# Optimization experiments

Hardware: AMD Instinct MI355X
Metric: run time of the kernel (lower is better)

The kernel has to match this reference:

```python
import jax, jax.numpy as jnp
import numpy as np

HEADS = 24
HEAD_DIM = 128
COND = 1024      # (512//8)*(512//8)*16//64
TXTLEN = 128
EPS = 1e-6


def setup_inputs() -> dict:
    key = jax.random.key(0)
    ks = jax.random.split(key, 16)
    S, D, R = 2176, 3072, 16
    f = lambda k, shp, s=1.0: jax.random.normal(k, shp, dtype=jnp.float32) * s
    return {
        "hidden_states": f(ks[0], (1, S, D)),
        "Wq": f(ks[1], (D, D), 0.02), "bq": f(ks[2], (D,), 0.02),
        "Wk": f(ks[3], (D, D), 0.02), "bk": f(ks[4], (D,), 0.02),
        "Wv": f(ks[5], (D, D), 0.02), "bv": f(ks[6], (D,), 0.02),
        "q_down": f(ks[7], (R, D), 1.0 / R), "q_up": f(ks[8], (D, R), 0.02),
        "k_down": f(ks[9], (R, D), 1.0 / R), "k_up": f(ks[10], (D, R), 0.02),
        "v_down": f(ks[11], (R, D), 1.0 / R), "v_up": f(ks[12], (D, R), 0.02),
        "norm_q_w": jnp.ones((HEAD_DIM,), jnp.float32),
        "norm_k_w": jnp.ones((HEAD_DIM,), jnp.float32),
        "rope_cos": f(ks[13], (S, HEAD_DIM)),
        "rope_sin": f(ks[14], (S, HEAD_DIM)),
    }


def _rms_norm(x, w):
    # per-head RMSNorm over head_dim
    var = jnp.mean(x * x, axis=-1, keepdims=True)
    return x * jax.lax.rsqrt(var + EPS) * w


def _apply_rope(x, cos, sin):
    # diffusers apply_rotary_emb, use_real=True, unbind_dim=-1 (interleaved pairs)
    xr = x.reshape(*x.shape[:-1], HEAD_DIM // 2, 2)
    x_rot = jnp.stack([-xr[..., 1], xr[..., 0]], axis=-1).reshape(x.shape)
    return x * cos[None, None] + x_rot * sin[None, None]


def _forward(hidden_states, Wq, bq, Wk, bk, Wv, bv,
             q_down, q_up, k_down, k_up, v_down, v_up,
             norm_q_w, norm_k_w, rope_cos, rope_sin):
    B, S, D = hidden_states.shape
    block = S - COND  # scaled_block_size

    # dense QKV projections
    q = hidden_states @ Wq.T + bq
    k = hidden_states @ Wk.T + bk
    v = hidden_states @ Wv.T + bv

    # LoRA on cond segment only (mask zeros all rows outside [block, block+COND))
    pos = jnp.arange(S)
    seg = ((pos >= block) & (pos < block + COND)).astype(hidden_states.dtype)[None, :, None]
    hm = hidden_states * seg
    # lora_weight=1.0, network_alpha/rank = 16/16 = 1.0
    q = q + (hm @ q_down.T) @ q_up.T
    k = k + (hm @ k_down.T) @ k_up.T
    v = v + (hm @ v_down.T) @ v_up.T

    # [B, H, S, hd]
    to_heads = lambda t: t.reshape(B, S, HEADS, HEAD_DIM).transpose(0, 2, 1, 3)
    q, k, v = to_heads(q), to_heads(k), to_heads(v)

    q = _rms_norm(q, norm_q_w)
    k = _rms_norm(k, norm_k_w)

    q = _apply_rope(q, rope_cos, rope_sin)
    k = _apply_rope(k, rope_cos, rope_sin)

    # additive mask: rows < block attend everything; cond rows (n_loras=1)
    # attend only their own cond block
    row, col = pos[:, None], pos[None, :]
    allowed = (row < block) | ((row >= block) & (col >= block))
    bias = jnp.where(allowed, 0.0, -1e20).astype(q.dtype)

    scale = 1.0 / np.sqrt(HEAD_DIM)
    scores = jnp.einsum("bhqd,bhkd->bhqk", q, k) * scale + bias
    attn = jax.nn.softmax(scores, axis=-1)
    out = jnp.einsum("bhqk,bhkd->bhqd", attn, v)

    out = out.transpose(0, 2, 1, 3).reshape(B, S, HEADS * HEAD_DIM)
    return out[:, :block, :]  # hidden_states (use_cond=False)


def reference(hidden_states, Wq, bq, Wk, bk, Wv, bv,
              q_down, q_up, k_down, k_up, v_down, v_up,
              norm_q_w, norm_k_w, rope_cos, rope_sin):
    return _forward(hidden_states, Wq, bq, Wk, bk, Wv, bv,
                    q_down, q_up, k_down, k_up, v_down, v_up,
                    norm_q_w, norm_k_w, rope_cos, rope_sin)
```

## Files before the change

kernel.cpp:

```cpp
#include <hip/hip_runtime.h>
#include <stdint.h>

#define Sq   2176
#define Dm   3072
#define NDm  9216
#define NH   24
#define HDm  128
#define BLKR 1152
#define KVH  1088
#define NT2  34

typedef __attribute__((ext_vector_type(8))) __bf16 bf16x8;
typedef __attribute__((ext_vector_type(4))) float f32x4;
typedef __attribute__((ext_vector_type(8))) unsigned short ushort8;

#define AS1 __attribute__((address_space(1)))
#define AS3 __attribute__((address_space(3)))

__device__ __forceinline__ unsigned short f2bf(float x) {
  unsigned u = __builtin_bit_cast(unsigned, x);
  u += 0x7FFFu + ((u >> 16) & 1u);
  return (unsigned short)(u >> 16);
}

__global__ void cvt_kernel(const float* __restrict__ src,
                           unsigned short* __restrict__ dst, int n8) {
  int i = blockIdx.x * blockDim.x + threadIdx.x;
  if (i >= n8) return;
  const float4* s4 = (const float4*)src + (size_t)i * 2;
  float4 a = s4[0], b = s4[1];
  ushort8 o;
  o[0]=f2bf(a.x); o[1]=f2bf(a.y); o[2]=f2bf(a.z); o[3]=f2bf(a.w);
  o[4]=f2bf(b.x); o[5]=f2bf(b.y); o[6]=f2bf(b.z); o[7]=f2bf(b.w);
  *((ushort8*)dst + i) = o;
}

__global__ void cvt3_kernel(const float* __restrict__ w0, const float* __restrict__ w1,
                            const float* __restrict__ w2,
                            unsigned short* __restrict__ dst, int n8) {
  int i = blockIdx.x * blockDim.x + threadIdx.x;
  if (i >= n8) return;
  const float* src = blockIdx.y == 0 ? w0 : (blockIdx.y == 1 ? w1 : w2);
  const float4* s4 = (const float4*)src + (size_t)i * 2;
  float4 a = s4[0], b = s4[1];
  ushort8 o;
  o[0]=f2bf(a.x); o[1]=f2bf(a.y); o[2]=f2bf(a.z); o[3]=f2bf(a.w);
  o[4]=f2bf(b.x); o[5]=f2bf(b.y); o[6]=f2bf(b.z); o[7]=f2bf(b.w);
  *((ushort8*)dst + (size_t)blockIdx.y * (Dm * (size_t)Dm / 8) + i) = o;
}

__global__ __launch_bounds__(256) void lorat_kernel(
    const float* __restrict__ hs,
    const float* __restrict__ k_down, const float* __restrict__ v_down,
    float* __restrict__ tkW, float* __restrict__ tvW) {
  int srow = BLKR + blockIdx.x;
  int t = threadIdx.x;
  __shared__ float hsl[Dm];
  __shared__ float tl[32];
  for (int e = t; e < Dm; e += 256) hsl[e] = hs[(size_t)srow * Dm + e];
  __syncthreads();
  int dot = t >> 3, part = t & 7;
  int mat = dot >> 4, j = dot & 15;
  const float* down = mat ? v_down : k_down;
  float p = 0.f;
  for (int e = part; e < Dm; e += 8) p += hsl[e] * down[j * Dm + e];
  p += __shfl_xor(p, 1, 64);
  p += __shfl_xor(p, 2, 64);
  p += __shfl_xor(p, 4, 64);
  if (part == 0) tl[dot] = p;
  __syncthreads();
  if (t < 16) tkW[(size_t)blockIdx.x * 16 + t] = tl[t];
  else if (t < 32) tvW[(size_t)blockIdx.x * 16 + (t - 16)] = tl[t];
}

__global__ __launch_bounds__(256, 4) void gemm_kernel(
    const unsigned short* __restrict__ A,
    const unsigned short* __restrict__ B,
    const float* __restrict__ bq, const float* __restrict__ bk,
    const float* __restrict__ bv,
    const float* __restrict__ tkW, const float* __restrict__ tvW,
    const float* __restrict__ kup, const float* __restrict__ vup,
    const float* __restrict__ nqw, const float* __restrict__ nkw,
    const float* __restrict__ rc, const float* __restrict__ rs,
    unsigned short* __restrict__ qh, unsigned short* __restrict__ kh,
    unsigned short* __restrict__ vtb) {
  __shared__ __attribute__((aligned(16))) unsigned short sm[17408];
  __shared__ float rsum[2][2][64];
  int t = threadIdx.x;
  int wid = t >> 6, lane = t & 63;
  int lr = lane & 15, lg = lane >> 4;
  int wr = wid >> 1, wc = wid & 1;

  int bid = blockIdx.x;
  int wg = (bid & 7) * 129 + (bid >> 3);
  int mt, nt;
  if (wg < 216) { nt = wg / 9; mt = wg % 9; }
  else { int r2 = wg - 216; nt = 24 + r2 / 17; mt = r2 % 17; }
  int m0 = mt * 128, n0 = nt * 128;

  f32x4 acc[4][4];
#pragma unroll
  for (int m = 0; m < 4; m++)
#pragma unroll
    for (int n = 0; n < 4; n++) acc[m][n] = (f32x4){0.f, 0.f, 0.f, 0.f};

  int tr = t >> 3;
  int uu = (t & 7) ^ (tr & 7);
  const unsigned short* pA = A + (size_t)(m0 + tr) * Dm + uu * 8;
  const unsigned short* pB = B + (size_t)(n0 + tr) * Dm + uu * 8;

  int lr7 = lr & 7;
  int baseA = (wr * 64 + lr) * 64;
  int baseB = (wc * 64 + lr) * 64;
  int d0 = (lg ^ lr7) * 8;
  int d1 = ((4 + lg) ^ lr7) * 8;

  for (int kt = 0; kt < Dm / 64; kt++) {
    const int ko = kt * 64;
#pragma unroll
    for (int c = 0; c < 4; c++) {
      __builtin_amdgcn_global_load_lds(
          (const AS1 void*)(pA + (size_t)c * 32 * Dm + ko),
          (AS3 void*)(&sm[c * 2048 + wid * 512]), 16, 0, 0);
      __builtin_amdgcn_global_load_lds(
          (const AS1 void*)(pB + (size_t)c * 32 * Dm + ko),
          (AS3 void*)(&sm[8192 + c * 2048 + wid * 512]), 16, 0, 0);
    }
    __syncthreads();

    bf16x8 a0[4], b0[4];
#pragma unroll
    for (int m = 0; m < 4; m++) a0[m] = *(const bf16x8*)&sm[baseA + m * 1024 + d0];
#pragma unroll
    for (int n = 0; n < 4; n++) b0[n] = *(const bf16x8*)&sm[8192 + baseB + n * 1024 + d0];
#pragma unroll
    for (int m = 0; m < 4; m++)
#pragma unroll
      for (int n = 0; n < 4; n++)
        acc[m][n] = __builtin_amdgcn_mfma_f32_16x16x32_bf16(a0[m], b0[n], acc[m][n], 0, 0, 0);

    bf16x8 a1[4], b1[4];
#pragma unroll
    for (int m = 0; m < 4; m++) a1[m] = *(const bf16x8*)&sm[baseA + m * 1024 + d1];
#pragma unroll
    for (int n = 0; n < 4; n++) b1[n] = *(const bf16x8*)&sm[8192 + baseB + n * 1024 + d1];
#pragma unroll
    for (int m = 0; m < 4; m++)
#pragma unroll
      for (int n = 0; n < 4; n++)
        acc[m][n] = __builtin_amdgcn_mfma_f32_16x16x32_bf16(a1[m], b1[n], acc[m][n], 0, 0, 0);
    __syncthreads();
  }

  int region = nt < 24 ? 0 : (nt < 48 ? 1 : 2);
  int h = region == 0 ? nt : (region == 1 ? nt - 24 : nt - 48);
  int dcol[4];
#pragma unroll
  for (int n = 0; n < 4; n++) dcol[n] = wc * 64 + n * 16 + lr;
  const float* bias = region == 0 ? bq : (region == 1 ? bk : bv);
#pragma unroll
  for (int n = 0; n < 4; n++) {
    float b = bias[h * 128 + dcol[n]];
#pragma unroll
    for (int m = 0; m < 4; m++)
#pragma unroll
      for (int i = 0; i < 4; i++) acc[m][n][i] += b;
  }

  if (region >= 1 && m0 >= BLKR) {
    const float* tW = region == 1 ? tkW : tvW;
    const float* up = region == 1 ? kup : vup;
    int rr = t >> 1, half = t & 1;
    const float* srcT = tW + ((size_t)(m0 - BLKR) + rr) * 16 + half * 8;
    const float* srcU = up + ((size_t)h * 128 + rr) * 16 + half * 8;
    ushort8 vT, vU;
#pragma unroll
    for (int u2 = 0; u2 < 8; u2++) { vT[u2] = f2bf(srcT[u2]); vU[u2] = f2bf(srcU[u2]); }
    ushort8 z = {0, 0, 0, 0, 0, 0, 0, 0};
    *(ushort8*)&sm[(rr * 8 + (half ^ (rr & 7))) * 8] = vT;
    *(ushort8*)&sm[(rr * 8 + ((2 + half) ^ (rr & 7))) * 8] = z;
    *(ushort8*)&sm[8192 + (rr * 8 + (half ^ (rr & 7))) * 8] = vU;
    *(ushort8*)&sm[8192 + (rr * 8 + ((2 + half) ^ (rr & 7))) * 8] = z;
    __syncthreads();
    bf16x8 a0[4], b0[4];
#pragma unroll
    for (int m = 0; m < 4; m++) a0[m] = *(const bf16x8*)&sm[baseA + m * 1024 + d0];
#pragma unroll
    for (int n = 0; n < 4; n++) b0[n] = *(const bf16x8*)&sm[8192 + baseB + n * 1024 + d0];
#pragma unroll
    for (int m = 0; m < 4; m++)
#pragma unroll
      for (int n = 0; n < 4; n++)
        acc[m][n] = __builtin_amdgcn_mfma_f32_16x16x32_bf16(a0[m], b0[n], acc[m][n], 0, 0, 0);
    __syncthreads();
  }

  if (region <= 1) {
    float part[4][4];
#pragma unroll
    for (int m = 0; m < 4; m++)
#pragma unroll
      for (int i = 0; i < 4; i++) {
        float p = acc[m][0][i] * acc[m][0][i] + acc[m][1][i] * acc[m][1][i]
                + acc[m][2][i] * acc[m][2][i] + acc[m][3][i] * acc[m][3][i];
#pragma unroll
        for (int d = 1; d < 16; d <<= 1) p += __shfl_xor(p, d, 64);
        part[m][i] = p;
      }
    if (lr == 0) {
#pragma unroll
      for (int m = 0; m < 4; m++)
#pragma unroll
        for (int i = 0; i < 4; i++) rsum[wr][wc][m * 16 + lg * 4 + i] = part[m][i];
    }
    __syncthreads();
    const float* nw = region == 0 ? nqw : nkw;
    float wv[4];
#pragma unroll
    for (int n = 0; n < 4; n++) wv[n] = nw[dcol[n]];
    unsigned short* dstb = region == 0 ? qh : kh;
    int srows = region == 0 ? BLKR : Sq;
#pragma unroll
    for (int m = 0; m < 4; m++)
#pragma unroll
      for (int i = 0; i < 4; i++) {
        int idx = m * 16 + lg * 4 + i;
        float s2 = rsum[wr][0][idx] + rsum[wr][1][idx];
        float rinv = rsqrtf(s2 * (1.f / 128.f) + 1e-6f);
        int r = m0 + wr * 64 + idx;
#pragma unroll
        for (int n = 0; n < 4; n++) {
          float xn = acc[m][n][i] * rinv * wv[n];
          float xp = __shfl_xor(xn, 1, 64);
          float c = rc[r * 128 + dcol[n]];
          float s = rs[r * 128 + dcol[n]];
          float rot = (dcol[n] & 1) ? xp : -xp;
          dstb[((size_t)h * srows + r) * 128 + dcol[n]] = f2bf(xn * c + rot * s);
        }
      }
  } else {
#pragma unroll
    for (int m = 0; m < 4; m++)
#pragma unroll
      for (int i = 0; i < 4; i++) {
        int rl = wr * 64 + m * 16 + lg * 4 + i;
#pragma unroll
        for (int n = 0; n < 4; n++)
          sm[dcol[n] * 136 + rl] = f2bf(acc[m][n][i]);
      }
    __syncthreads();
    int d = t >> 1, rc0 = (t & 1) * 64;
    unsigned short* dv = vtb + ((size_t)h * 128 + d) * Sq + m0 + rc0;
#pragma unroll
    for (int u = 0; u < 8; u++)
      *(ushort8*)(dv + u * 8) = *(const ushort8*)&sm[d * 136 + rc0 + u * 8];
  }
}

__global__ __launch_bounds__(256) void attn_kernel(
    const unsigned short* __restrict__ qh,
    const unsigned short* __restrict__ kh,
    const unsigned short* __restrict__ vt,
    float* __restrict__ accW,
    float* __restrict__ lW) {
  int bid = blockIdx.x;
  int wg = (bid & 7) * 108 + (bid >> 3);
  int h = wg / 36, rem = wg % 36;
  int qt = rem >> 1, split = rem & 1;
  int q0 = qt * 64;
  int k0 = split * KVH;

  int t = threadIdx.x;
  int w = t >> 6, lane = t & 63;
  int lr = lane & 15, lg = lane >> 4;

  __shared__ __attribute__((aligned(16))) unsigned short kLds[2][32 * 128];
  __shared__ __attribute__((aligned(16))) unsigned short vLds[2][128 * 32];

  const unsigned short* qb = qh + ((size_t)h * BLKR + q0 + w * 16) * 128;
  bf16x8 aq[4];
#pragma unroll
  for (int m = 0; m < 4; m++)
    aq[m] = *(const bf16x8*)(qb + (size_t)lr * 128 + m * 32 + lg * 8);

  const unsigned short* kh_h = kh + ((size_t)h * Sq + k0) * 128;
  const unsigned short* vt_h = vt + (size_t)h * 128 * Sq + k0;

  const unsigned short* srcK[2];
  const unsigned short* srcV[2];
  int kDst[2], vDst[2];
#pragma unroll
  for (int c = 0; c < 2; c++) {
    int u = c * 256 + t;
    int rK = u >> 4, sK = u & 15;
    srcK[c] = kh_h + (size_t)rK * 128 + ((sK ^ (rK & 7)) * 8);
    kDst[c] = u * 8;
    int rV = u >> 2, sV = u & 3;
    srcV[c] = vt_h + (size_t)rV * Sq + ((sV ^ (rV & 3)) * 8);
    vDst[c] = u * 8;
  }

  auto stage = [&](int kt, int buf) {
#pragma unroll
    for (int c = 0; c < 2; c++)
      __builtin_amdgcn_global_load_lds(
          (const AS1 void*)(srcK[c] + (size_t)kt * 4096),
          (AS3 void*)(&kLds[buf][kDst[c]]), 16, 0, 0);
#pragma unroll
    for (int c = 0; c < 2; c++)
      __builtin_amdgcn_global_load_lds(
          (const AS1 void*)(srcV[c] + (size_t)kt * 32),
          (AS3 void*)(&vLds[buf][vDst[c]]), 16, 0, 0);
  };

  f32x4 acc[8];
#pragma unroll
  for (int o = 0; o < 8; o++) acc[o] = (f32x4){0.f, 0.f, 0.f, 0.f};
  float lsum = 0.f;
  const float sc = 0.08838834764831845f;
  const float L2E = 1.4426950408889634f;
  const float ea = sc * L2E, eb = -10.0f * L2E;

  int lr7 = lr & 7, lr3 = lr & 3;
  int adLo = ((((lg & 1) << 1)) * 16 + lr) * 4;
  int adHi = adLo + 64;
  bool hiKb = (lg & 2) != 0;

  auto compute = [&](int buf) {
    const unsigned short* kbuf = kLds[buf];
    const unsigned short* vbuf = vLds[buf];
    f32x4 s2[2];
    s2[0] = (f32x4){0.f, 0.f, 0.f, 0.f};
    s2[1] = (f32x4){0.f, 0.f, 0.f, 0.f};
    __builtin_amdgcn_s_setprio(1);
#pragma unroll
    for (int kb = 0; kb < 2; kb++)
#pragma unroll
      for (int m = 0; m < 4; m++) {
        bf16x8 kf = *(const bf16x8*)&kbuf[(kb * 16 + lr) * 128 + ((m * 4 + lg) ^ lr7) * 8];
        s2[kb] = __builtin_amdgcn_mfma_f32_16x16x32_bf16(kf, aq[m], s2[kb], 0, 0, 0);
      }
    __builtin_amdgcn_s_setprio(0);
    unsigned pk0[2], pk1[2];
#pragma unroll
    for (int kb = 0; kb < 2; kb++) {
      float p0 = exp2f(fmaf(s2[kb][0], ea, eb));
      float p1 = exp2f(fmaf(s2[kb][1], ea, eb));
      float p2 = exp2f(fmaf(s2[kb][2], ea, eb));
      float p3 = exp2f(fmaf(s2[kb][3], ea, eb));
      lsum += (p0 + p1) + (p2 + p3);
      unsigned r0, r1;
      asm("v_cvt_pk_bf16_f32 %0, %1, %2" : "=v"(r0) : "v"(p0), "v"(p1));
      asm("v_cvt_pk_bf16_f32 %0, %1, %2" : "=v"(r1) : "v"(p2), "v"(p3));
      if (kb == 0) { pk0[0] = r0; pk0[1] = r1; }
      else         { pk1[0] = r0; pk1[1] = r1; }
    }
    int a00 = __builtin_amdgcn_ds_bpermute(adLo, (int)pk0[0]);
    int a01 = __builtin_amdgcn_ds_bpermute(adLo, (int)pk0[1]);
    int a10 = __builtin_amdgcn_ds_bpermute(adLo, (int)pk1[0]);
    int a11 = __builtin_amdgcn_ds_bpermute(adLo, (int)pk1[1]);
    int b00 = __builtin_amdgcn_ds_bpermute(adHi, (int)pk0[0]);
    int b01 = __builtin_amdgcn_ds_bpermute(adHi, (int)pk0[1]);
    int b10 = __builtin_amdgcn_ds_bpermute(adHi, (int)pk1[0]);
    int b11 = __builtin_amdgcn_ds_bpermute(adHi, (int)pk1[1]);
    int4 pw;
    pw.x = hiKb ? a10 : a00;
    pw.y = hiKb ? a11 : a01;
    pw.z = hiKb ? b10 : b00;
    pw.w = hiKb ? b11 : b01;
    bf16x8 pfrag = __builtin_bit_cast(bf16x8, pw);
    __builtin_amdgcn_s_setprio(1);
#pragma unroll
    for (int o = 0; o < 8; o++) {
      bf16x8 vf = *(const bf16x8*)&vbuf[(o * 16 + lr) * 32 + (lg ^ lr3) * 8];
      acc[o] = __builtin_amdgcn_mfma_f32_16x16x32_bf16(vf, pfrag, acc[o], 0, 0, 0);
    }
    __builtin_amdgcn_s_setprio(0);
  };

  stage(0, 0);
  __syncthreads();
  for (int kt = 0; kt < NT2; kt += 2) {
    stage(kt + 1, 1);
    compute(0);
    __syncthreads();
    if (kt + 2 < NT2) stage(kt + 2, 0);
    compute(1);
    __syncthreads();
  }

  lsum += __shfl_xor(lsum, 16, 64);
  lsum += __shfl_xor(lsum, 32, 64);

  float* accP = accW + (size_t)split * BLKR * 3072;
  size_t rowOff = (size_t)(q0 + w * 16 + lr) * 3072 + h * 128;
#pragma unroll
  for (int o = 0; o < 8; o++)
    *(f32x4*)&accP[rowOff + o * 16 + lg * 4] = acc[o];
  if (lg == 0) {
    float* lP = lW + (size_t)split * NH * BLKR + (size_t)h * BLKR;
    lP[q0 + w * 16 + lr] = lsum;
  }
}

__global__ __launch_bounds__(256) void normalize_kernel(
    const float* __restrict__ accW, const float* __restrict__ lW,
    float* __restrict__ out) {
  int idx = blockIdx.x * 256 + threadIdx.x;
  int r = idx / 384, rem = idx % 384;
  int c = rem * 8, h = c >> 7;
  const float4* a0 = (const float4*)(accW + (size_t)r * 3072 + c);
  const float4* a1 = (const float4*)(accW + (size_t)BLKR * 3072 + (size_t)r * 3072 + c);
  float l = lW[(size_t)h * BLKR + r] + lW[(size_t)NH * BLKR + (size_t)h * BLKR + r];
  float inv = 1.0f / l;
  float4 v0 = a0[0], v1 = a0[1], u0 = a1[0], u1 = a1[1];
  float4 o0, o1;
  o0.x = (v0.x + u0.x) * inv; o0.y = (v0.y + u0.y) * inv;
  o0.z = (v0.z + u0.z) * inv; o0.w = (v0.w + u0.w) * inv;
  o1.x = (v1.x + u1.x) * inv; o1.y = (v1.y + u1.y) * inv;
  o1.z = (v1.z + u1.z) * inv; o1.w = (v1.w + u1.w) * inv;
  float4* op = (float4*)(out + (size_t)r * 3072 + c);
  op[0] = o0; op[1] = o1;
}

extern "C" void kernel_launch(void* const* d_in, const int* in_sizes, int n_in,
                              void* d_out, int out_size, void* d_ws, size_t ws_size,
                              hipStream_t stream) {
  const float* hs  = (const float*)d_in[0];
  const float* Wq  = (const float*)d_in[1];
  const float* bq  = (const float*)d_in[2];
  const float* Wk  = (const float*)d_in[3];
  const float* bk  = (const float*)d_in[4];
  const float* Wv  = (const float*)d_in[5];
  const float* bv  = (const float*)d_in[6];
  const float* k_down = (const float*)d_in[9];
  const float* k_up   = (const float*)d_in[10];
  const float* v_down = (const float*)d_in[11];
  const float* v_up   = (const float*)d_in[12];
  const float* nqw = (const float*)d_in[13];
  const float* nkw = (const float*)d_in[14];
  const float* rc  = (const float*)d_in[15];
  const float* rsn = (const float*)d_in[16];
  float* out = (float*)d_out;

  char* ws = (char*)d_ws;
  unsigned short* hsb = (unsigned short*)(ws + 0);
  unsigned short* wb  = (unsigned short*)(ws + 13369344);
  float* accW = (float*)(ws + 69992448);
  float* lW   = (float*)(ws + 98304000);
  float* tkW  = (float*)(ws + 98525184);
  float* tvW  = (float*)(ws + 98590720);
  unsigned short* qh  = (unsigned short*)(ws + 150208512);
  unsigned short* kh  = (unsigned short*)(ws + 157286400);
  unsigned short* vtb = (unsigned short*)(ws + 170655744);

  const int n8_hs = Sq * Dm / 8;
  const int n8_w  = Dm * Dm / 8;
  cvt_kernel<<<dim3((n8_hs + 255) / 256), 256, 0, stream>>>(hs, hsb, n8_hs);
  cvt3_kernel<<<dim3((n8_w + 255) / 256, 3), 256, 0, stream>>>(Wq, Wk, Wv, wb, n8_w);
  lorat_kernel<<<dim3(Sq - BLKR), 256, 0, stream>>>(hs, k_down, v_down, tkW, tvW);

  gemm_kernel<<<dim3(1032), 256, 0, stream>>>(hsb, wb, bq, bk, bv,
                                              tkW, tvW, k_up, v_up,
                                              nqw, nkw, rc, rsn, qh, kh, vtb);
  attn_kernel<<<dim3(2 * 18 * NH), 256, 0, stream>>>(qh, kh, vtb, accW, lW);
  normalize_kernel<<<dim3(BLKR * 3072 / 8 / 256), 256, 0, stream>>>(accW, lW, out);
}
```

Before: 304.0 us.

## Load K/V fragments directly from global memory instead of LDS double-buffering

The attention kernel stops staging K and V tiles into shared memory with async global-to-LDS loads and barriers. Each wave now loads its own K and V MFMA fragments straight from global memory into registers every iteration. This removes the LDS traffic and block-wide syncs, but each of the four waves re-reads the same K/V data from global/L2, and there is no explicit prefetch to hide load latency.

```diff
diff --git a/kernel.cpp b/kernel.cpp
--- a/kernel.cpp
+++ b/kernel.cpp
@@ -274,44 +274,14 @@
   int w = t >> 6, lane = t & 63;
   int lr = lane & 15, lg = lane >> 4;
 
-  __shared__ __attribute__((aligned(16))) unsigned short kLds[2][32 * 128];
-  __shared__ __attribute__((aligned(16))) unsigned short vLds[2][128 * 32];
-
   const unsigned short* qb = qh + ((size_t)h * BLKR + q0 + w * 16) * 128;
   bf16x8 aq[4];
 #pragma unroll
   for (int m = 0; m < 4; m++)
     aq[m] = *(const bf16x8*)(qb + (size_t)lr * 128 + m * 32 + lg * 8);
 
-  const unsigned short* kh_h = kh + ((size_t)h * Sq + k0) * 128;
-  const unsigned short* vt_h = vt + (size_t)h * 128 * Sq + k0;
-
-  const unsigned short* srcK[2];
-  const unsigned short* srcV[2];
-  int kDst[2], vDst[2];
-#pragma unroll
-  for (int c = 0; c < 2; c++) {
-    int u = c * 256 + t;
-    int rK = u >> 4, sK = u & 15;
-    srcK[c] = kh_h + (size_t)rK * 128 + ((sK ^ (rK & 7)) * 8);
-    kDst[c] = u * 8;
-    int rV = u >> 2, sV = u & 3;
-    srcV[c] = vt_h + (size_t)rV * Sq + ((sV ^ (rV & 3)) * 8);
-    vDst[c] = u * 8;
-  }
-
-  auto stage = [&](int kt, int buf) {
-#pragma unroll
-    for (int c = 0; c < 2; c++)
-      __builtin_amdgcn_global_load_lds(
-          (const AS1 void*)(srcK[c] + (size_t)kt * 4096),
-          (AS3 void*)(&kLds[buf][kDst[c]]), 16, 0, 0);
-#pragma unroll
-    for (int c = 0; c < 2; c++)
-      __builtin_amdgcn_global_load_lds(
-          (const AS1 void*)(srcV[c] + (size_t)kt * 32),
-          (AS3 void*)(&vLds[buf][vDst[c]]), 16, 0, 0);
-  };
+  const unsigned short* kp = kh + ((size_t)h * Sq + k0 + lr) * 128 + lg * 8;
+  const unsigned short* vp = vt + ((size_t)h * 128 + lr) * Sq + k0 + lg * 8;
 
   f32x4 acc[8];
 #pragma unroll
@@ -321,14 +291,24 @@
   const float L2E = 1.4426950408889634f;
   const float ea = sc * L2E, eb = -10.0f * L2E;
 
-  int lr7 = lr & 7, lr3 = lr & 3;
   int adLo = ((((lg & 1) << 1)) * 16 + lr) * 4;
   int adHi = adLo + 64;
   bool hiKb = (lg & 2) != 0;
 
-  auto compute = [&](int buf) {
-    const unsigned short* kbuf = kLds[buf];
-    const unsigned short* vbuf = vLds[buf];
+  for (int kt = 0; kt < NT2; kt++) {
+    const unsigned short* kpt = kp + (size_t)kt * 32 * 128;
+    const unsigned short* vpt = vp + kt * 32;
+    bf16x8 kf[2][4];
+#pragma unroll
+    for (int kb = 0; kb < 2; kb++)
+#pragma unroll
+      for (int m = 0; m < 4; m++)
+        kf[kb][m] = *(const bf16x8*)(kpt + kb * 16 * 128 + m * 32);
+    bf16x8 vf[8];
+#pragma unroll
+    for (int o = 0; o < 8; o++)
+      vf[o] = *(const bf16x8*)(vpt + (size_t)o * 16 * Sq);
+
     f32x4 s2[2];
     s2[0] = (f32x4){0.f, 0.f, 0.f, 0.f};
     s2[1] = (f32x4){0.f, 0.f, 0.f, 0.f};
@@ -336,11 +316,10 @@
 #pragma unroll
     for (int kb = 0; kb < 2; kb++)
 #pragma unroll
-      for (int m = 0; m < 4; m++) {
-        bf16x8 kf = *(const bf16x8*)&kbuf[(kb * 16 + lr) * 128 + ((m * 4 + lg) ^ lr7) * 8];
-        s2[kb] = __builtin_amdgcn_mfma_f32_16x16x32_bf16(kf, aq[m], s2[kb], 0, 0, 0);
-      }
+      for (int m = 0; m < 4; m++)
+        s2[kb] = __builtin_amdgcn_mfma_f32_16x16x32_bf16(kf[kb][m], aq[m], s2[kb], 0, 0, 0);
     __builtin_amdgcn_s_setprio(0);
+
     unsigned pk0[2], pk1[2];
 #pragma unroll
     for (int kb = 0; kb < 2; kb++) {
@@ -371,22 +350,9 @@
     bf16x8 pfrag = __builtin_bit_cast(bf16x8, pw);
     __builtin_amdgcn_s_setprio(1);
 #pragma unroll
-    for (int o = 0; o < 8; o++) {
-      bf16x8 vf = *(const bf16x8*)&vbuf[(o * 16 + lr) * 32 + (lg ^ lr3) * 8];
-      acc[o] = __builtin_amdgcn_mfma_f32_16x16x32_bf16(vf, pfrag, acc[o], 0, 0, 0);
-    }
+    for (int o = 0; o < 8; o++)
+      acc[o] = __builtin_amdgcn_mfma_f32_16x16x32_bf16(vf[o], pfrag, acc[o], 0, 0, 0);
     __builtin_amdgcn_s_setprio(0);
-  };
-
-  stage(0, 0);
-  __syncthreads();
-  for (int kt = 0; kt < NT2; kt += 2) {
-    stage(kt + 1, 1);
-    compute(0);
-    __syncthreads();
-    if (kt + 2 < NT2) stage(kt + 2, 0);
-    compute(1);
-    __syncthreads();
   }
 
   lsum += __shfl_xor(lsum, 16, 64);
```

Result: slower. 488.1 us (+60.5%).

## Double attention query tile per workgroup to reuse K/V LDS tiles

Applied to the files above, without the earlier changes.

Each attention workgroup now processes 128 query rows instead of 64, with each wave holding two 16-row Q sub-tiles. Every K and V fragment loaded from LDS feeds two MFMAs, which halves K/V global and LDS traffic per query. The grid shrinks from 864 to 432 workgroups, which lowers occupancy and CU fill on a 256-CU part and raises register pressure from the doubled accumulators.

```diff
diff --git a/kernel.cpp b/kernel.cpp
--- a/kernel.cpp
+++ b/kernel.cpp
@@ -264,10 +264,10 @@
     float* __restrict__ accW,
     float* __restrict__ lW) {
   int bid = blockIdx.x;
-  int wg = (bid & 7) * 108 + (bid >> 3);
-  int h = wg / 36, rem = wg % 36;
+  int wg = (bid & 7) * 54 + (bid >> 3);
+  int h = wg / 18, rem = wg % 18;
   int qt = rem >> 1, split = rem & 1;
-  int q0 = qt * 64;
+  int q0 = qt * 128;
   int k0 = split * KVH;
 
   int t = threadIdx.x;
@@ -277,11 +277,13 @@
   __shared__ __attribute__((aligned(16))) unsigned short kLds[2][32 * 128];
   __shared__ __attribute__((aligned(16))) unsigned short vLds[2][128 * 32];
 
-  const unsigned short* qb = qh + ((size_t)h * BLKR + q0 + w * 16) * 128;
-  bf16x8 aq[4];
-#pragma unroll
-  for (int m = 0; m < 4; m++)
-    aq[m] = *(const bf16x8*)(qb + (size_t)lr * 128 + m * 32 + lg * 8);
+  const unsigned short* qb = qh + ((size_t)h * BLKR + q0 + w * 32) * 128;
+  bf16x8 aq[2][4];
+#pragma unroll
+  for (int qs = 0; qs < 2; qs++)
+#pragma unroll
+    for (int m = 0; m < 4; m++)
+      aq[qs][m] = *(const bf16x8*)(qb + (size_t)(qs * 16 + lr) * 128 + m * 32 + lg * 8);
 
   const unsigned short* kh_h = kh + ((size_t)h * Sq + k0) * 128;
   const unsigned short* vt_h = vt + (size_t)h * 128 * Sq + k0;
@@ -313,10 +315,12 @@
           (AS3 void*)(&vLds[buf][vDst[c]]), 16, 0, 0);
   };
 
-  f32x4 acc[8];
-#pragma unroll
-  for (int o = 0; o < 8; o++) acc[o] = (f32x4){0.f, 0.f, 0.f, 0.f};
-  float lsum = 0.f;
+  f32x4 acc[2][8];
+#pragma unroll
+  for (int qs = 0; qs < 2; qs++)
+#pragma unroll
+    for (int o = 0; o < 8; o++) acc[qs][o] = (f32x4){0.f, 0.f, 0.f, 0.f};
+  float lsum[2] = {0.f, 0.f};
   const float sc = 0.08838834764831845f;
   const float L2E = 1.4426950408889634f;
   const float ea = sc * L2E, eb = -10.0f * L2E;
@@ -329,51 +333,66 @@
   auto compute = [&](int buf) {
     const unsigned short* kbuf = kLds[buf];
     const unsigned short* vbuf = vLds[buf];
-    f32x4 s2[2];
-    s2[0] = (f32x4){0.f, 0.f, 0.f, 0.f};
-    s2[1] = (f32x4){0.f, 0.f, 0.f, 0.f};
+    f32x4 s2[2][2];
+#pragma unroll
+    for (int qs = 0; qs < 2; qs++) {
+      s2[qs][0] = (f32x4){0.f, 0.f, 0.f, 0.f};
+      s2[qs][1] = (f32x4){0.f, 0.f, 0.f, 0.f};
+    }
     __builtin_amdgcn_s_setprio(1);
 #pragma unroll
-    for (int kb = 0; kb < 2; kb++)
-#pragma unroll
-      for (int m = 0; m < 4; m++) {
-        bf16x8 kf = *(const bf16x8*)&kbuf[(kb * 16 + lr) * 128 + ((m * 4 + lg) ^ lr7) * 8];
-        s2[kb] = __builtin_amdgcn_mfma_f32_16x16x32_bf16(kf, aq[m], s2[kb], 0, 0, 0);
+    for (int kb = 0; kb < 2; kb++) {
+      bf16x8 kf[4];
+#pragma unroll
+      for (int m = 0; m < 4; m++)
+        kf[m] = *(const bf16x8*)&kbuf[(kb * 16 + lr) * 128 + ((m * 4 + lg) ^ lr7) * 8];
+#pragma unroll
+      for (int qs = 0; qs < 2; qs++)
+#pragma unroll
+        for (int m = 0; m < 4; m++)
+          s2[qs][kb] = __builtin_amdgcn_mfma_f32_16x16x32_bf16(kf[m], aq[qs][m], s2[qs][kb], 0, 0, 0);
+    }
+    __builtin_amdgcn_s_setprio(0);
+
+    bf16x8 pfrag[2];
+#pragma unroll
+    for (int qs = 0; qs < 2; qs++) {
+      unsigned pk0[2], pk1[2];
+#pragma unroll
+      for (int kb = 0; kb < 2; kb++) {
+        float p0 = exp2f(fmaf(s2[qs][kb][0], ea, eb));
+        float p1 = exp2f(fmaf(s2[qs][kb][1], ea, eb));
+        float p2 = exp2f(fmaf(s2[qs][kb][2], ea, eb));
+        float p3 = exp2f(fmaf(s2[qs][kb][3], ea, eb));
+        lsum[qs] += (p0 + p1) + (p2 + p3);
+        unsigned r0, r1;
+        asm("v_cvt_pk_bf16_f32 %0, %1, %2" : "=v"(r0) : "v"(p0), "v"(p1));
+        asm("v_cvt_pk_bf16_f32 %0, %1, %2" : "=v"(r1) : "v"(p2), "v"(p3));
+        if (kb == 0) { pk0[0] = r0; pk0[1] = r1; }
+        else         { pk1[0] = r0; pk1[1] = r1; }
       }
-    __builtin_amdgcn_s_setprio(0);
-    unsigned pk0[2], pk1[2];
-#pragma unroll
-    for (int kb = 0; kb < 2; kb++) {
-      float p0 = exp2f(fmaf(s2[kb][0], ea, eb));
-      float p1 = exp2f(fmaf(s2[kb][1], ea, eb));
-      float p2 = exp2f(fmaf(s2[kb][2], ea, eb));
-      float p3 = exp2f(fmaf(s2[kb][3], ea, eb));
-      lsum += (p0 + p1) + (p2 + p3);
-      unsigned r0, r1;
-      asm("v_cvt_pk_bf16_f32 %0, %1, %2" : "=v"(r0) : "v"(p0), "v"(p1));
-      asm("v_cvt_pk_bf16_f32 %0, %1, %2" : "=v"(r1) : "v"(p2), "v"(p3));
-      if (kb == 0) { pk0[0] = r0; pk0[1] = r1; }
-      else         { pk1[0] = r0; pk1[1] = r1; }
-    }
-    int a00 = __builtin_amdgcn_ds_bpermute(adLo, (int)pk0[0]);
-    int a01 = __builtin_amdgcn_ds_bpermute(adLo, (int)pk0[1]);
-    int a10 = __builtin_amdgcn_ds_bpermute(adLo, (int)pk1[0]);
-    int a11 = __builtin_amdgcn_ds_bpermute(adLo, (int)pk1[1]);
-    int b00 = __builtin_amdgcn_ds_bpermute(adHi, (int)pk0[0]);
-    int b01 = __builtin_amdgcn_ds_bpermute(adHi, (int)pk0[1]);
-    int b10 = __builtin_amdgcn_ds_bpermute(adHi, (int)pk1[0]);
-    int b11 = __builtin_amdgcn_ds_bpermute(adHi, (int)pk1[1]);
-    int4 pw;
-    pw.x = hiKb ? a10 : a00;
-    pw.y = hiKb ? a11 : a01;
-    pw.z = hiKb ? b10 : b00;
-    pw.w = hiKb ? b11 : b01;
-    bf16x8 pfrag = __builtin_bit_cast(bf16x8, pw);
+      int a00 = __builtin_amdgcn_ds_bpermute(adLo, (int)pk0[0]);
+      int a01 = __builtin_amdgcn_ds_bpermute(adLo, (int)pk0[1]);
+      int a10 = __builtin_amdgcn_ds_bpermute(adLo, (int)pk1[0]);
+      int a11 = __builtin_amdgcn_ds_bpermute(adLo, (int)pk1[1]);
+      int b00 = __builtin_amdgcn_ds_bpermute(adHi, (int)pk0[0]);
+      int b01 = __builtin_amdgcn_ds_bpermute(adHi, (int)pk0[1]);
+      int b10 = __builtin_amdgcn_ds_bpermute(adHi, (int)pk1[0]);
+      int b11 = __builtin_amdgcn_ds_bpermute(adHi, (int)pk1[1]);
+      int4 pw;
+      pw.x = hiKb ? a10 : a00;
+      pw.y = hiKb ? a11 : a01;
+      pw.z = hiKb ? b10 : b00;
+      pw.w = hiKb ? b11 : b01;
+      pfrag[qs] = __builtin_bit_cast(bf16x8, pw);
+    }
+
     __builtin_amdgcn_s_setprio(1);
 #pragma unroll
     for (int o = 0; o < 8; o++) {
       bf16x8 vf = *(const bf16x8*)&vbuf[(o * 16 + lr) * 32 + (lg ^ lr3) * 8];
-      acc[o] = __builtin_amdgcn_mfma_f32_16x16x32_bf16(vf, pfrag, acc[o], 0, 0, 0);
+      acc[0][o] = __builtin_amdgcn_mfma_f32_16x16x32_bf16(vf, pfrag[0], acc[0][o], 0, 0, 0);
+      acc[1][o] = __builtin_amdgcn_mfma_f32_16x16x32_bf16(vf, pfrag[1], acc[1][o], 0, 0, 0);
     }
     __builtin_amdgcn_s_setprio(0);
   };
@@ -389,17 +408,24 @@
     __syncthreads();
   }
 
-  lsum += __shfl_xor(lsum, 16, 64);
-  lsum += __shfl_xor(lsum, 32, 64);
+#pragma unroll
+  for (int qs = 0; qs < 2; qs++) {
+    lsum[qs] += __shfl_xor(lsum[qs], 16, 64);
+    lsum[qs] += __shfl_xor(lsum[qs], 32, 64);
+  }
 
   float* accP = accW + (size_t)split * BLKR * 3072;
-  size_t rowOff = (size_t)(q0 + w * 16 + lr) * 3072 + h * 128;
-#pragma unroll
-  for (int o = 0; o < 8; o++)
-    *(f32x4*)&accP[rowOff + o * 16 + lg * 4] = acc[o];
+#pragma unroll
+  for (int qs = 0; qs < 2; qs++) {
+    size_t rowOff = (size_t)(q0 + w * 32 + qs * 16 + lr) * 3072 + h * 128;
+#pragma unroll
+    for (int o = 0; o < 8; o++)
+      *(f32x4*)&accP[rowOff + o * 16 + lg * 4] = acc[qs][o];
+  }
   if (lg == 0) {
     float* lP = lW + (size_t)split * NH * BLKR + (size_t)h * BLKR;
-    lP[q0 + w * 16 + lr] = lsum;
+    lP[q0 + w * 32 + lr] = lsum[0];
+    lP[q0 + w * 32 + 16 + lr] = lsum[1];
   }
 }
 
@@ -463,6 +489,6 @@
   gemm_kernel<<<dim3(1032), 256, 0, stream>>>(hsb, wb, bq, bk, bv,
                                               tkW, tvW, k_up, v_up,
                                               nqw, nkw, rc, rsn, qh, kh, vtb);
-  attn_kernel<<<dim3(2 * 18 * NH), 256, 0, stream>>>(qh, kh, vtb, accW, lW);
+  attn_kernel<<<dim3(2 * 9 * NH), 256, 0, stream>>>(qh, kh, vtb, accW, lW);
   normalize_kernel<<<dim3(BLKR * 3072 / 8 / 256), 256, 0, stream>>>(accW, lW, out);
 }
```

New measurement: 313.0 us. +2.9%, slower.

## Fuse prep kernels into one launch and store split-attention partials in bf16

Applied to the files above, without the earlier changes.

Merges the hidden-state conversion, the three weight conversions and the LoRA down-projection into a single prep kernel. The LoRA part now handles four rows per block so each down-projection load is reused four times. The attention kernel writes its split-K partial accumulators as bf16 instead of fp32, halving partial-output traffic, and the normalize kernel reads them back as bf16. This removes two launches and some memory traffic, at the cost of extra rounding error in the partial sums.

```diff
diff --git a/kernel.cpp b/kernel.cpp
--- a/kernel.cpp
+++ b/kernel.cpp
@@ -9,6 +9,11 @@
 #define BLKR 1152
 #define KVH  1088
 #define NT2  34
+#define N8HS 835584
+#define N8W  1179648
+#define NB_CVT   3264
+#define NB_W     13824
+#define NB_LORAT 256
 
 typedef __attribute__((ext_vector_type(8))) __bf16 bf16x8;
 typedef __attribute__((ext_vector_type(4))) float f32x4;
@@ -22,55 +27,75 @@
   u += 0x7FFFu + ((u >> 16) & 1u);
   return (unsigned short)(u >> 16);
 }
-
-__global__ void cvt_kernel(const float* __restrict__ src,
-                           unsigned short* __restrict__ dst, int n8) {
-  int i = blockIdx.x * blockDim.x + threadIdx.x;
-  if (i >= n8) return;
-  const float4* s4 = (const float4*)src + (size_t)i * 2;
-  float4 a = s4[0], b = s4[1];
-  ushort8 o;
-  o[0]=f2bf(a.x); o[1]=f2bf(a.y); o[2]=f2bf(a.z); o[3]=f2bf(a.w);
-  o[4]=f2bf(b.x); o[5]=f2bf(b.y); o[6]=f2bf(b.z); o[7]=f2bf(b.w);
-  *((ushort8*)dst + i) = o;
-}
-
-__global__ void cvt3_kernel(const float* __restrict__ w0, const float* __restrict__ w1,
-                            const float* __restrict__ w2,
-                            unsigned short* __restrict__ dst, int n8) {
-  int i = blockIdx.x * blockDim.x + threadIdx.x;
-  if (i >= n8) return;
-  const float* src = blockIdx.y == 0 ? w0 : (blockIdx.y == 1 ? w1 : w2);
-  const float4* s4 = (const float4*)src + (size_t)i * 2;
-  float4 a = s4[0], b = s4[1];
-  ushort8 o;
-  o[0]=f2bf(a.x); o[1]=f2bf(a.y); o[2]=f2bf(a.z); o[3]=f2bf(a.w);
-  o[4]=f2bf(b.x); o[5]=f2bf(b.y); o[6]=f2bf(b.z); o[7]=f2bf(b.w);
-  *((ushort8*)dst + (size_t)blockIdx.y * (Dm * (size_t)Dm / 8) + i) = o;
-}
-
-__global__ __launch_bounds__(256) void lorat_kernel(
+__device__ __forceinline__ float bf2f(unsigned short x) {
+  return __builtin_bit_cast(float, (unsigned)x << 16);
+}
+
+__global__ __launch_bounds__(256) void prep_kernel(
     const float* __restrict__ hs,
+    const float* __restrict__ w0, const float* __restrict__ w1,
+    const float* __restrict__ w2,
     const float* __restrict__ k_down, const float* __restrict__ v_down,
+    unsigned short* __restrict__ hsb, unsigned short* __restrict__ wb,
     float* __restrict__ tkW, float* __restrict__ tvW) {
-  int srow = BLKR + blockIdx.x;
-  int t = threadIdx.x;
-  __shared__ float hsl[Dm];
-  __shared__ float tl[32];
-  for (int e = t; e < Dm; e += 256) hsl[e] = hs[(size_t)srow * Dm + e];
+  __shared__ float hsl[4 * Dm];
+  __shared__ float tl[4][32];
+  int bid = blockIdx.x, t = threadIdx.x;
+
+  if (bid < NB_CVT) {
+    int i = bid * 256 + t;
+    const float4* s4 = (const float4*)hs + (size_t)i * 2;
+    float4 a = s4[0], b = s4[1];
+    ushort8 o;
+    o[0]=f2bf(a.x); o[1]=f2bf(a.y); o[2]=f2bf(a.z); o[3]=f2bf(a.w);
+    o[4]=f2bf(b.x); o[5]=f2bf(b.y); o[6]=f2bf(b.z); o[7]=f2bf(b.w);
+    *((ushort8*)hsb + i) = o;
+    return;
+  }
+  if (bid < NB_CVT + NB_W) {
+    int idx = (bid - NB_CVT) * 256 + t;
+    int mat = idx < N8W ? 0 : (idx < 2 * N8W ? 1 : 2);
+    int i = idx - mat * N8W;
+    const float* src = mat == 0 ? w0 : (mat == 1 ? w1 : w2);
+    const float4* s4 = (const float4*)src + (size_t)i * 2;
+    float4 a = s4[0], b = s4[1];
+    ushort8 o;
+    o[0]=f2bf(a.x); o[1]=f2bf(a.y); o[2]=f2bf(a.z); o[3]=f2bf(a.w);
+    o[4]=f2bf(b.x); o[5]=f2bf(b.y); o[6]=f2bf(b.z); o[7]=f2bf(b.w);
+    *((ushort8*)wb + (size_t)mat * (Dm * (size_t)Dm / 8) + i) = o;
+    return;
+  }
+  int bid2 = bid - (NB_CVT + NB_W);
+  int r0 = bid2 * 4;
+  for (int e = t; e < 4 * Dm; e += 256)
+    hsl[e] = hs[((size_t)BLKR + r0) * Dm + e];
   __syncthreads();
   int dot = t >> 3, part = t & 7;
   int mat = dot >> 4, j = dot & 15;
   const float* down = mat ? v_down : k_down;
-  float p = 0.f;
-  for (int e = part; e < Dm; e += 8) p += hsl[e] * down[j * Dm + e];
-  p += __shfl_xor(p, 1, 64);
-  p += __shfl_xor(p, 2, 64);
-  p += __shfl_xor(p, 4, 64);
-  if (part == 0) tl[dot] = p;
+  float p0 = 0.f, p1 = 0.f, p2 = 0.f, p3 = 0.f;
+  for (int e = part; e < Dm; e += 8) {
+    float dv = down[j * Dm + e];
+    p0 = fmaf(hsl[e], dv, p0);
+    p1 = fmaf(hsl[Dm + e], dv, p1);
+    p2 = fmaf(hsl[2 * Dm + e], dv, p2);
+    p3 = fmaf(hsl[3 * Dm + e], dv, p3);
+  }
+#pragma unroll
+  for (int d = 1; d < 8; d <<= 1) {
+    p0 += __shfl_xor(p0, d, 64);
+    p1 += __shfl_xor(p1, d, 64);
+    p2 += __shfl_xor(p2, d, 64);
+    p3 += __shfl_xor(p3, d, 64);
+  }
+  if (part == 0) { tl[0][dot] = p0; tl[1][dot] = p1; tl[2][dot] = p2; tl[3][dot] = p3; }
   __syncthreads();
-  if (t < 16) tkW[(size_t)blockIdx.x * 16 + t] = tl[t];
-  else if (t < 32) tvW[(size_t)blockIdx.x * 16 + (t - 16)] = tl[t];
+  if (t < 128) {
+    int rr = t >> 5, jj = t & 31;
+    float v = tl[rr][jj];
+    if (jj < 16) tkW[(size_t)(r0 + rr) * 16 + jj] = v;
+    else         tvW[(size_t)(r0 + rr) * 16 + (jj - 16)] = v;
+  }
 }
 
 __global__ __launch_bounds__(256, 4) void gemm_kernel(
@@ -261,7 +286,7 @@
     const unsigned short* __restrict__ qh,
     const unsigned short* __restrict__ kh,
     const unsigned short* __restrict__ vt,
-    float* __restrict__ accW,
+    unsigned short* __restrict__ accW,
     float* __restrict__ lW) {
   int bid = blockIdx.x;
   int wg = (bid & 7) * 108 + (bid >> 3);
@@ -392,11 +417,14 @@
   lsum += __shfl_xor(lsum, 16, 64);
   lsum += __shfl_xor(lsum, 32, 64);
 
-  float* accP = accW + (size_t)split * BLKR * 3072;
+  unsigned short* accP = accW + (size_t)split * BLKR * 3072;
   size_t rowOff = (size_t)(q0 + w * 16 + lr) * 3072 + h * 128;
 #pragma unroll
-  for (int o = 0; o < 8; o++)
-    *(f32x4*)&accP[rowOff + o * 16 + lg * 4] = acc[o];
+  for (int o = 0; o < 8; o++) {
+    ushort4 o4 = make_ushort4(f2bf(acc[o][0]), f2bf(acc[o][1]),
+                              f2bf(acc[o][2]), f2bf(acc[o][3]));
+    *(ushort4*)&accP[rowOff + o * 16 + lg * 4] = o4;
+  }
   if (lg == 0) {
     float* lP = lW + (size_t)split * NH * BLKR + (size_t)h * BLKR;
     lP[q0 + w * 16 + lr] = lsum;
@@ -404,21 +432,24 @@
 }
 
 __global__ __launch_bounds__(256) void normalize_kernel(
-    const float* __restrict__ accW, const float* __restrict__ lW,
+    const unsigned short* __restrict__ accW, const float* __restrict__ lW,
     float* __restrict__ out) {
   int idx = blockIdx.x * 256 + threadIdx.x;
   int r = idx / 384, rem = idx % 384;
   int c = rem * 8, h = c >> 7;
-  const float4* a0 = (const float4*)(accW + (size_t)r * 3072 + c);
-  const float4* a1 = (const float4*)(accW + (size_t)BLKR * 3072 + (size_t)r * 3072 + c);
+  ushort8 u0 = *(const ushort8*)(accW + (size_t)r * 3072 + c);
+  ushort8 u1 = *(const ushort8*)(accW + (size_t)BLKR * 3072 + (size_t)r * 3072 + c);
   float l = lW[(size_t)h * BLKR + r] + lW[(size_t)NH * BLKR + (size_t)h * BLKR + r];
   float inv = 1.0f / l;
-  float4 v0 = a0[0], v1 = a0[1], u0 = a1[0], u1 = a1[1];
   float4 o0, o1;
-  o0.x = (v0.x + u0.x) * inv; o0.y = (v0.y + u0.y) * inv;
-  o0.z = (v0.z + u0.z) * inv; o0.w = (v0.w + u0.w) * inv;
-  o1.x = (v1.x + u1.x) * inv; o1.y = (v1.y + u1.y) * inv;
-  o1.z = (v1.z + u1.z) * inv; o1.w = (v1.w + u1.w) * inv;
+  o0.x = (bf2f(u0[0]) + bf2f(u1[0])) * inv;
+  o0.y = (bf2f(u0[1]) + bf2f(u1[1])) * inv;
+  o0.z = (bf2f(u0[2]) + bf2f(u1[2])) * inv;
+  o0.w = (bf2f(u0[3]) + bf2f(u1[3])) * inv;
+  o1.x = (bf2f(u0[4]) + bf2f(u1[4])) * inv;
+  o1.y = (bf2f(u0[5]) + bf2f(u1[5])) * inv;
+  o1.z = (bf2f(u0[6]) + bf2f(u1[6])) * inv;
+  o1.w = (bf2f(u0[7]) + bf2f(u1[7])) * inv;
   float4* op = (float4*)(out + (size_t)r * 3072 + c);
   op[0] = o0; op[1] = o1;
 }
@@ -446,7 +477,7 @@
   char* ws = (char*)d_ws;
   unsigned short* hsb = (unsigned short*)(ws + 0);
   unsigned short* wb  = (unsigned short*)(ws + 13369344);
-  float* accW = (float*)(ws + 69992448);
+  unsigned short* accW = (unsigned short*)(ws + 69992448);
   float* lW   = (float*)(ws + 98304000);
   float* tkW  = (float*)(ws + 98525184);
   float* tvW  = (float*)(ws + 98590720);
@@ -454,11 +485,8 @@
   unsigned short* kh  = (unsigned short*)(ws + 157286400);
   unsigned short* vtb = (unsigned short*)(ws + 170655744);
 
-  const int n8_hs = Sq * Dm / 8;
-  const int n8_w  = Dm * Dm / 8;
-  cvt_kernel<<<dim3((n8_hs + 255) / 256), 256, 0, stream>>>(hs, hsb, n8_hs);
-  cvt3_kernel<<<dim3((n8_w + 255) / 256, 3), 256, 0, stream>>>(Wq, Wk, Wv, wb, n8_w);
-  lorat_kernel<<<dim3(Sq - BLKR), 256, 0, stream>>>(hs, k_down, v_down, tkW, tvW);
+  prep_kernel<<<dim3(NB_CVT + NB_W + NB_LORAT), 256, 0, stream>>>(
+      hs, Wq, Wk, Wv, k_down, v_down, hsb, wb, tkW, tvW);
 
   gemm_kernel<<<dim3(1032), 256, 0, stream>>>(hsb, wb, bq, bk, bv,
                                               tkW, tvW, k_up, v_up,
```

After: 297.6 us. -2.1%, faster.
